# Kernel optimization log

Measured on AMD Instinct MI355X. Metric: run time of the kernel, lower is better.

## Reference

```python
import jax, jax.numpy as jnp
import numpy as np

N_NODES = 2048
N_EDGES = 49152
R_MAX = 6.0
NUM_BASIS = 8
N_LAYERS = 4
AVG_NEIGH = 24.0
MUL_S, MUL_V = 32, 16                 # hidden irreps = 32x0e + 16x1o
N_SC_OUT = MUL_S + MUL_V              # 48 scalar channels before gate (32 scalars + 16 gates)
HID = MUL_S + 3 * MUL_V               # 80 = hidden feature dim
RAD_H = 64
# tp path weight sizes: (0e x 0e -> 0e), (1o x 1o -> 0e), (0e x 1o -> 1o), (1o x 0e -> 1o), (1o x 2e -> 1o)
N1 = MUL_S * N_SC_OUT; N2 = MUL_V * N_SC_OUT; N3 = MUL_S * MUL_V; N4 = MUL_V * MUL_V; N5 = MUL_V * MUL_V
WNUM = N1 + N2 + N3 + N4 + N5         # 3328

# orthonormal symmetric-traceless basis for real l=2 (order: xy, yz, z2, xz, x2-y2)
_s2 = 1.0 / np.sqrt(2.0); _s6 = 1.0 / np.sqrt(6.0)
_Q = np.zeros((5, 3, 3), np.float32)
_Q[0, 0, 1] = _Q[0, 1, 0] = _s2
_Q[1, 1, 2] = _Q[1, 2, 1] = _s2
_Q[2, 0, 0] = _Q[2, 1, 1] = -_s6; _Q[2, 2, 2] = 2 * _s6
_Q[3, 0, 2] = _Q[3, 2, 0] = _s2
_Q[4, 0, 0] = _s2; _Q[4, 1, 1] = -_s2
Q2 = jnp.asarray(_Q)


def _sph(d):
    # component-normalized real spherical harmonics of unit vectors d [E,3]
    x, y, z = d[:, 0], d[:, 1], d[:, 2]
    y1 = jnp.sqrt(3.0) * d
    c = jnp.sqrt(15.0)
    y2 = jnp.stack([c * x * y, c * y * z, 0.5 * jnp.sqrt(5.0) * (3 * z * z - 1.0),
                    c * x * z, 0.5 * c * (x * x - y * y)], -1)
    return y1, y2


def _bessel_cutoff(r):
    # Bessel radial basis * polynomial cutoff (p=6); r [E,1]
    n = jnp.arange(1, NUM_BASIS + 1, dtype=jnp.float32)
    rbf = jnp.sqrt(2.0 / R_MAX) * jnp.sin(n * jnp.pi * r / R_MAX) / r
    u = r / R_MAX
    f = (1.0 - 28.0 * u ** 6 + 48.0 * u ** 7 - 21.0 * u ** 8) * (u < 1.0)
    return rbf * f


def _lin(h, Ws, Wv):
    # e3nn Linear hidden -> hidden (per-irrep channel mixing, fan-in normalized)
    s = h[:, :MUL_S] @ Ws / jnp.sqrt(float(MUL_S))
    v = jnp.einsum('nui,uw->nwi', h[:, MUL_S:].reshape(-1, MUL_V, 3), Wv) / jnp.sqrt(float(MUL_V))
    return jnp.concatenate([s, v.reshape(-1, 3 * MUL_V)], -1)


def reference(x, pos, edge_index, embed_w, proj_w, lin_ws, lin_wv, sc_ws, sc_wv,
              mlp_w1, mlp_b1, mlp_w2, mlp_b2, mlp_w3, mlp_b3):
    src, dst = edge_index[0], edge_index[1]
    rel = pos[dst] - pos[src]                                   # pos_i - pos_j
    r = jnp.maximum(jnp.linalg.norm(rel, axis=-1, keepdims=True), 1e-6)
    d = rel / r
    y1, y2 = _sph(d)
    rbf = _bessel_cutoff(r)                                     # [E, 8]
    # embed: only 0e->0e path exists; 1o part starts at zero
    h = jnp.concatenate([x @ embed_w / jnp.sqrt(16.0),
                         jnp.zeros((x.shape[0], 3 * MUL_V), x.dtype)], -1)
    for l in range(N_LAYERS):
        x_res = h
        x_self = _lin(h, sc_ws[l], sc_wv[l])
        hx = _lin(h, lin_ws[l], lin_wv[l])
        # radial MLP -> per-edge tensor-product weights
        f = jax.nn.silu(rbf @ mlp_w1[l] + mlp_b1[l])
        f = jax.nn.silu(f @ mlp_w2[l] + mlp_b2[l])
        w = f @ mlp_w3[l] + mlp_b3[l]                           # [E, WNUM]
        o = 0
        w1 = w[:, o:o + N1].reshape(-1, MUL_S, N_SC_OUT); o += N1
        w2 = w[:, o:o + N2].reshape(-1, MUL_V, N_SC_OUT); o += N2
        w3 = w[:, o:o + N3].reshape(-1, MUL_S, MUL_V);    o += N3
        w4 = w[:, o:o + N4].reshape(-1, MUL_V, MUL_V);    o += N4
        w5 = w[:, o:o + N5].reshape(-1, MUL_V, MUL_V)
        s_j = hx[src, :MUL_S]
        v_j = hx[src, MUL_S:].reshape(-1, MUL_V, 3)
        # scalar outputs: (0e x 0e -> 0e) and (1o x 1o -> 0e)
        p2 = jnp.einsum('eui,ei->eu', v_j, y1) / jnp.sqrt(3.0)
        out_s = (jnp.einsum('eu,euw->ew', s_j, w1) + jnp.einsum('eu,euw->ew', p2, w2)) / jnp.sqrt(48.0)
        # vector outputs: (0e x 1o -> 1o), (1o x 0e -> 1o), (1o x 2e -> 1o)
        q3 = jnp.einsum('eu,ei->eui', s_j, y1)
        q5 = jnp.sqrt(3.0 / 5.0) * jnp.einsum('eui,em,mij->euj', v_j, y2, Q2)
        out_v = (jnp.einsum('eui,euw->ewi', q3, w3) + jnp.einsum('eui,euw->ewi', v_j, w4)
                 + jnp.einsum('eui,euw->ewi', q5, w5)) / jnp.sqrt(64.0)
        msg = jnp.concatenate([out_s, out_v.reshape(-1, 3 * MUL_V)], -1)   # [E, 96]
        agg = jax.ops.segment_sum(msg, dst, num_segments=N_NODES) / jnp.sqrt(AVG_NEIGH)
        # Gate: silu on scalars, sigmoid gates scale 1o channels
        sc = jax.nn.silu(agg[:, :MUL_S])
        g = jax.nn.sigmoid(agg[:, MUL_S:MUL_S + MUL_V])
        vec = agg[:, MUL_S + MUL_V:].reshape(-1, MUL_V, 3) * g[:, :, None]
        h = x_res + x_self + jnp.concatenate([sc, vec.reshape(-1, 3 * MUL_V)], -1)
    return h[:, :MUL_S] @ proj_w / jnp.sqrt(float(MUL_S))


def setup_inputs() -> dict:
    key = jax.random.key(0)
    ks = jax.random.split(key, 16)
    nrm = jax.random.normal
    return {
        'x': nrm(ks[0], (N_NODES, 16), jnp.float32),
        'pos': 2.0 * nrm(ks[1], (N_NODES, 3), jnp.float32),
        'edge_index': jax.random.randint(ks[2], (2, N_EDGES), 0, N_NODES),
        'embed_w': nrm(ks[3], (16, MUL_S), jnp.float32),
        'proj_w': nrm(ks[4], (MUL_S, 32), jnp.float32),
        'lin_ws': nrm(ks[5], (N_LAYERS, MUL_S, MUL_S), jnp.float32),
        'lin_wv': nrm(ks[6], (N_LAYERS, MUL_V, MUL_V), jnp.float32),
        'sc_ws': nrm(ks[7], (N_LAYERS, MUL_S, MUL_S), jnp.float32),
        'sc_wv': nrm(ks[8], (N_LAYERS, MUL_V, MUL_V), jnp.float32),
        'mlp_w1': nrm(ks[9], (N_LAYERS, NUM_BASIS, RAD_H), jnp.float32) / np.sqrt(NUM_BASIS),
        'mlp_b1': jnp.zeros((N_LAYERS, RAD_H), jnp.float32),
        'mlp_w2': nrm(ks[10], (N_LAYERS, RAD_H, RAD_H), jnp.float32) / np.sqrt(RAD_H),
        'mlp_b2': jnp.zeros((N_LAYERS, RAD_H), jnp.float32),
        'mlp_w3': nrm(ks[11], (N_LAYERS, RAD_H, WNUM), jnp.float32) / np.sqrt(RAD_H),
        'mlp_b3': jnp.zeros((N_LAYERS, WNUM), jnp.float32),
    }
```

## Files before the change

kernel.cpp:

```cpp
#include <hip/hip_runtime.h>
#include <math.h>

#define NN 2048
#define NE 49152
#define WNUM 3328

typedef __attribute__((ext_vector_type(8))) _Float16 half8;
typedef __attribute__((ext_vector_type(4))) float f32x4;

__device__ __forceinline__ float silu_f(float x){ return x / (1.0f + expf(-x)); }
__device__ __forceinline__ float sigm_f(float x){ return 1.0f / (1.0f + expf(-x)); }

__global__ void geom_kernel(const float* __restrict__ pos, const int* __restrict__ ei,
                            float* __restrict__ egeo, int* __restrict__ cnt) {
  int e = blockIdx.x * 256 + threadIdx.x;
  if (e >= NE) return;
  int s = ei[e], d = ei[NE + e];
  atomicAdd(&cnt[d], 1);
  float rx = pos[d*3+0] - pos[s*3+0];
  float ry = pos[d*3+1] - pos[s*3+1];
  float rz = pos[d*3+2] - pos[s*3+2];
  float r = sqrtf(rx*rx + ry*ry + rz*rz);
  r = fmaxf(r, 1e-6f);
  float x = rx / r, y = ry / r, z = rz / r;
  const float s3 = 1.7320508075688772f;
  const float c15 = 3.872983346207417f;
  float y2_0 = c15 * x * y;
  float y2_1 = c15 * y * z;
  float y2_2 = 1.118033988749895f * (3.0f*z*z - 1.0f);
  float y2_3 = c15 * x * z;
  float y2_4 = 1.9364916731037085f * (x*x - y*y);
  const float q2 = 0.7071067811865476f;
  const float q6 = 0.4082482904638631f;
  float* g = egeo + (size_t)e * 20;
  g[0] = s3 * x; g[1] = s3 * y; g[2] = s3 * z;
  g[3+0] = -q6*y2_2 + q2*y2_4;
  g[3+1] =  q2*y2_0;
  g[3+2] =  q2*y2_3;
  g[3+3] =  q2*y2_0;
  g[3+4] = -q6*y2_2 - q2*y2_4;
  g[3+5] =  q2*y2_1;
  g[3+6] =  q2*y2_3;
  g[3+7] =  q2*y2_1;
  g[3+8] =  2.0f*q6*y2_2;
  float u = r / 6.0f;
  float fc = 0.0f;
  if (u < 1.0f) {
    float u2=u*u, u3=u2*u, u6=u3*u3, u7=u6*u, u8=u7*u;
    fc = 1.0f - 28.0f*u6 + 48.0f*u7 - 21.0f*u8;
  }
  const float pref = 0.5773502691896258f;
  const float pi6 = 0.5235987755982988f;
  #pragma unroll
  for (int n = 1; n <= 8; n++) {
    g[12 + n - 1] = pref * sinf((float)n * pi6 * r) / r * fc;
  }
}

__global__ void scan_kernel(const int* __restrict__ cnt, int* __restrict__ offs,
                            int* __restrict__ cursor) {
  __shared__ int part[256];
  int t = threadIdx.x;
  int local[8];
  int s = 0;
  #pragma unroll
  for (int j = 0; j < 8; j++) { local[j] = s; s += cnt[t*8 + j]; }
  part[t] = s;
  __syncthreads();
  for (int off = 1; off < 256; off <<= 1) {
    int v = part[t];
    int add = (t >= off) ? part[t - off] : 0;
    __syncthreads();
    part[t] = v + add;
    __syncthreads();
  }
  int excl = (t == 0) ? 0 : part[t-1];
  #pragma unroll
  for (int j = 0; j < 8; j++) {
    int o = excl + local[j];
    offs[t*8 + j] = o;
    cursor[t*8 + j] = o;
  }
  if (t == 255) offs[2048] = part[255];
}

__global__ void scatter_kernel(const int* __restrict__ ei, int* __restrict__ cursor,
                               int* __restrict__ epos) {
  int e = blockIdx.x * 256 + threadIdx.x;
  if (e >= NE) return;
  int d = ei[NE + e];
  int p = atomicAdd(&cursor[d], 1);
  epos[e] = p;
}

__global__ void conv_w3_kernel(const float* __restrict__ w3g, _Float16* __restrict__ w3h) {
  int tid = blockIdx.x * 256 + threadIdx.x;
  if (tid >= 16 * WNUM) return;
  int n = tid % WNUM;
  int lq = tid / WNUM;
  int quad = lq & 3, l = lq >> 2;
  const float* src = w3g + (size_t)l * 64 * WNUM + n;
  int idx = n >> 4, L = n & 15;
  _Float16* dst = w3h + ((size_t)(l * 208 + idx) * 2) * 512 + (quad*16 + L) * 8;
  half8 h0, h1;
  #pragma unroll
  for (int j = 0; j < 8; j++) {
    h0[j] = (_Float16)src[(size_t)(quad*8 + j) * WNUM];
    h1[j] = (_Float16)src[(size_t)(32 + quad*8 + j) * WNUM];
  }
  *(half8*)(dst)       = h0;
  *(half8*)(dst + 512) = h1;
}

#define NBR1 (NE/16)
__global__ void radial_all_kernel(const float* __restrict__ egeo,
                                  const float* __restrict__ w1, const float* __restrict__ b1,
                                  const float* __restrict__ w2, const float* __restrict__ b2,
                                  _Float16* __restrict__ f_h) {
  __shared__ float h1s[16][64];
  int l = blockIdx.x / NBR1;
  int bb = blockIdx.x % NBR1;
  int ty = threadIdx.x >> 6, dk = threadIdx.x & 63;
  int e0b = bb * 16 + ty * 4;
  const float* w1l = w1 + (size_t)l * 8 * 64;
  const float* w2l = w2 + (size_t)l * 64 * 64;
  _Float16* fl = f_h + (size_t)l * NE * 64;
  float b1v = b1[l*64 + dk];
  #pragma unroll
  for (int k = 0; k < 4; ++k) {
    const float* rb = egeo + (size_t)(e0b + k) * 20 + 12;
    float acc = b1v;
    #pragma unroll
    for (int j = 0; j < 8; j++) acc += rb[j] * w1l[j*64 + dk];
    h1s[ty*4 + k][dk] = silu_f(acc);
  }
  __syncthreads();
  float b2v = b2[l*64 + dk];
  float o0 = b2v, o1 = b2v, o2 = b2v, o3 = b2v;
  #pragma unroll 8
  for (int j = 0; j < 64; ++j) {
    float w = w2l[j*64 + dk];
    o0 += h1s[ty*4+0][j] * w;
    o1 += h1s[ty*4+1][j] * w;
    o2 += h1s[ty*4+2][j] * w;
    o3 += h1s[ty*4+3][j] * w;
  }
  fl[(size_t)(e0b+0)*64 + dk] = (_Float16)silu_f(o0);
  fl[(size_t)(e0b+1)*64 + dk] = (_Float16)silu_f(o1);
  fl[(size_t)(e0b+2)*64 + dk] = (_Float16)silu_f(o2);
  fl[(size_t)(e0b+3)*64 + dk] = (_Float16)silu_f(o3);
}

__global__ void embed_prep_kernel(const float* __restrict__ x, const float* __restrict__ ew,
                                  const float* __restrict__ lws0, const float* __restrict__ sws0,
                                  float* __restrict__ h, float* __restrict__ hx,
                                  float* __restrict__ xself) {
  __shared__ float hs[8][32];
  int t = threadIdx.x;
  int nl = t >> 5, c = t & 31;
  int n = blockIdx.x * 8 + nl;
  float v = 0.0f;
  #pragma unroll
  for (int j = 0; j < 16; j++) v += x[n*16 + j] * ew[j*32 + c];
  v *= 0.25f;
  hs[nl][c] = v;
  h[(size_t)n*80 + c] = v;
  for (int idx = t; idx < 8*48; idx += 256) {
    int nn = blockIdx.x * 8 + idx / 48;
    h[(size_t)nn*80 + 32 + idx % 48] = 0.0f;
  }
  __syncthreads();
  for (int idx = t; idx < 2*8*80; idx += 256) {
    int which = idx / 640, r = idx % 640;
    int nl2 = r / 80, cc = r % 80;
    int n2 = blockIdx.x * 8 + nl2;
    float o = 0.0f;
    if (cc < 32) {
      const float* W = which ? sws0 : lws0;
      #pragma unroll 8
      for (int u = 0; u < 32; u++) o += hs[nl2][u] * W[u*32 + cc];
      o *= 0.17677669529663687f;
    }
    (which ? xself : hx)[(size_t)n2*80 + cc] = o;
  }
}

__launch_bounds__(256, 2)
__global__ void edge_msg_kernel(const int* __restrict__ ei, const float* __restrict__ egeo,
                                const _Float16* __restrict__ f_h,
                                const float* __restrict__ hx,
                                const _Float16* __restrict__ w3h,
                                const float* __restrict__ b3g,
                                const int* __restrict__ epos,
                                float* __restrict__ msg, int l) {
  __shared__ float smem[15616];
  __shared__ int eposS[64];
  float* sT    = smem;
  float* p2T   = smem + 2048;
  float* q3T   = smem + 3072;
  float* vT    = smem + 6144;
  float* q5T   = smem + 9216;
  float* biasL = smem + 12288;
  float* poolA = smem;
  float* poolB = smem + 3072;
  float* poolC = smem + 6144;

  const int t = threadIdx.x;
  const int e0 = blockIdx.x * 64;
  const float* b3l = b3g + (size_t)l * WNUM;

  for (int i = t; i < WNUM; i += 256) biasL[i] = b3l[i];
  if (t < 64) eposS[t] = epos[e0 + t];
  for (int idx = t; idx < 64*80; idx += 256) {
    int e = idx / 80, c = idx % 80;
    int src = ei[e0 + e];
    float val = hx[(size_t)src*80 + c];
    if (c < 32) sT[c*64 + e] = val; else vT[(c-32)*64 + e] = val;
  }
  __syncthreads();
  for (int idx = t; idx < 64*16; idx += 256) {
    int u = idx >> 6, e = idx & 63;
    const float* g = &egeo[(size_t)(e0+e)*20];
    float a = vT[(u*3)*64+e]*g[0] + vT[(u*3+1)*64+e]*g[1] + vT[(u*3+2)*64+e]*g[2];
    p2T[u*64 + e] = a * 0.5773502691896258f;
  }
  for (int idx = t; idx < 64*48; idx += 256) {
    int o = idx >> 6, e = idx & 63;
    int u = o / 3, jj = o % 3;
    const float* g = &egeo[(size_t)(e0+e)*20];
    q3T[o*64 + e] = sT[u*64 + e] * g[jj];
    float a = vT[(u*3)*64+e]*g[3+jj] + vT[(u*3+1)*64+e]*g[6+jj] + vT[(u*3+2)*64+e]*g[9+jj];
    q5T[o*64 + e] = a * 0.7745966692414834f;
  }

  const int wv = t >> 6, lane = t & 63, L = lane & 15, quad = lane >> 4;
  const int qb = quad * 4;

  half8 Ah[4][2];
  #pragma unroll
  for (int g = 0; g < 4; ++g) {
    const half8* fA = (const half8*)(f_h + (size_t)(e0 + g*16 + L)*64);
    Ah[g][0] = fA[quad];
    Ah[g][1] = fA[4 + quad];
  }
  __syncthreads();

  const _Float16* wb = w3h + (size_t)l * 208 * 1024 + lane * 8;
  half8 pb0[4], pb1[4];
  float bs[4];

#define PRIME(START)                                                          \
  { _Pragma("unroll")                                                         \
    for (int _s = 0; _s < 4; ++_s) {                                          \
      const _Float16* _wn = wb + (size_t)((START) + _s) * 1024;               \
      pb0[_s] = *(const half8*)_wn;                                           \
      pb1[_s] = *(const half8*)(_wn + 512);                                   \
      bs[_s] = biasL[((START) + _s)*16 + L];                                  \
    } }

#define GCORE(IDX, CO, OKCOND)                                                \
  f32x4 a0, a1, a2, a3;                                                       \
  { half8 _B0 = pb0[(CO)&3], _B1 = pb1[(CO)&3];                               \
    float _bb = bs[(CO)&3];                                                   \
    if (OKCOND) {                                                             \
      const _Float16* _wn = wb + (size_t)((IDX) + 4) * 1024;                  \
      pb0[(CO)&3] = *(const half8*)_wn;                                       \
      pb1[(CO)&3] = *(const half8*)(_wn + 512);                               \
      bs[(CO)&3] = biasL[((IDX) + 4)*16 + L];                                 \
    }                                                                         \
    a0 = (f32x4){_bb,_bb,_bb,_bb}; a1 = a0; a2 = a0; a3 = a0;                 \
    a0 = __builtin_amdgcn_mfma_f32_16x16x32_f16(Ah[0][0], _B0, a0, 0,0,0);    \
    a0 = __builtin_amdgcn_mfma_f32_16x16x32_f16(Ah[0][1], _B1, a0, 0,0,0);    \
    a1 = __builtin_amdgcn_mfma_f32_16x16x32_f16(Ah[1][0], _B0, a1, 0,0,0);    \
    a1 = __builtin_amdgcn_mfma_f32_16x16x32_f16(Ah[1][1], _B1, a1, 0,0,0);    \
    a2 = __builtin_amdgcn_mfma_f32_16x16x32_f16(Ah[2][0], _B0, a2, 0,0,0);    \
    a2 = __builtin_amdgcn_mfma_f32_16x16x32_f16(Ah[2][1], _B1, a2, 0,0,0);    \
    a3 = __builtin_amdgcn_mfma_f32_16x16x32_f16(Ah[3][0], _B0, a3, 0,0,0);    \
    a3 = __builtin_amdgcn_mfma_f32_16x16x32_f16(Ah[3][1], _B1, a3, 0,0,0);    \
  }

  const float S48 = 0.14433756729740645f;
  const float S64 = 0.125f;

  if (wv <= 1) {
    f32x4 ms[4][3];
    #pragma unroll
    for (int g = 0; g < 4; ++g)
      #pragma unroll
      for (int j = 0; j < 3; ++j) ms[g][j] = (f32x4){0,0,0,0};
    const int ustart = wv * 16, istart = wv * 48, iend = istart + 48;
    PRIME(istart);
    for (int u4 = 0; u4 < 16; u4 += 4) {
      #pragma unroll
      for (int uu = 0; uu < 4; ++uu) {
        const int u = u4 + uu;
        f32x4 f0 = *(const f32x4*)&sT[(ustart+u)*64 + qb];
        f32x4 f1 = *(const f32x4*)&sT[(ustart+u)*64 + 16 + qb];
        f32x4 f2 = *(const f32x4*)&sT[(ustart+u)*64 + 32 + qb];
        f32x4 f3 = *(const f32x4*)&sT[(ustart+u)*64 + 48 + qb];
        #pragma unroll
        for (int j = 0; j < 3; ++j) {
          const int CO = uu*3 + j;
          const int idx = istart + u4*3 + CO;
          GCORE(idx, CO, idx + 4 < iend);
          ms[0][j] += f0*a0; ms[1][j] += f1*a1; ms[2][j] += f2*a2; ms[3][j] += f3*a3;
        }
      }
    }
    float* pool = (wv == 0) ? poolA : poolB;
    __syncthreads();
    #pragma unroll
    for (int g = 0; g < 4; ++g)
      #pragma unroll
      for (int j = 0; j < 3; ++j)
        #pragma unroll
        for (int r = 0; r < 4; ++r)
          pool[(g*16 + qb + r)*48 + j*16 + L] = ms[g][j][r];
    __syncthreads();
  } else if (wv == 2) {
    f32x4 ms[4][3], mv[4][3];
    #pragma unroll
    for (int g = 0; g < 4; ++g)
      #pragma unroll
      for (int j = 0; j < 3; ++j) { ms[g][j] = (f32x4){0,0,0,0}; mv[g][j] = (f32x4){0,0,0,0}; }
    PRIME(96);
    for (int u4 = 0; u4 < 16; u4 += 4) {
      #pragma unroll
      for (int uu = 0; uu < 4; ++uu) {
        const int u = u4 + uu;
        f32x4 f0 = *(const f32x4*)&p2T[u*64 + qb];
        f32x4 f1 = *(const f32x4*)&p2T[u*64 + 16 + qb];
        f32x4 f2 = *(const f32x4*)&p2T[u*64 + 32 + qb];
        f32x4 f3 = *(const f32x4*)&p2T[u*64 + 48 + qb];
        #pragma unroll
        for (int j = 0; j < 3; ++j) {
          const int CO = uu*3 + j;
          const int idx = 96 + u4*3 + CO;
          GCORE(idx, CO, idx + 4 < 144);
          ms[0][j] += f0*a0; ms[1][j] += f1*a1; ms[2][j] += f2*a2; ms[3][j] += f3*a3;
        }
      }
    }
    PRIME(176);
    for (int u4 = 0; u4 < 16; u4 += 4) {
      #pragma unroll
      for (int uu = 0; uu < 4; ++uu) {
        const int u = u4 + uu;
        const int idx = 176 + u;
        GCORE(idx, uu, idx + 4 < 192);
        #pragma unroll
        for (int i = 0; i < 3; ++i) {
          mv[0][i] += *(const f32x4*)&vT[(u*3+i)*64 + qb]      * a0;
          mv[1][i] += *(const f32x4*)&vT[(u*3+i)*64 + 16 + qb] * a1;
          mv[2][i] += *(const f32x4*)&vT[(u*3+i)*64 + 32 + qb] * a2;
          mv[3][i] += *(const f32x4*)&vT[(u*3+i)*64 + 48 + qb] * a3;
        }
      }
    }
    __syncthreads();
    #pragma unroll
    for (int g = 0; g < 4; ++g)
      #pragma unroll
      for (int i = 0; i < 3; ++i)
        #pragma unroll
        for (int r = 0; r < 4; ++r)
          poolC[(g*16 + qb + r)*48 + i*16 + L] = mv[g][i][r];
    __syncthreads();
    #pragma unroll
    for (int g = 0; g < 4; ++g) {
      #pragma unroll
      for (int r = 0; r < 4; ++r) {
        const int eb = g*16 + qb + r;
        float* mp = msg + (size_t)eposS[eb]*96;
        #pragma unroll
        for (int j = 0; j < 3; ++j)
          mp[j*16 + L] = (ms[g][j][r] + poolA[eb*48 + j*16 + L] + poolB[eb*48 + j*16 + L]) * S48;
      }
    }
  } else {
    f32x4 mv[4][3];
    #pragma unroll
    for (int g = 0; g < 4; ++g)
      #pragma unroll
      for (int i = 0; i < 3; ++i) mv[g][i] = (f32x4){0,0,0,0};
    PRIME(144);
    for (int u4 = 0; u4 < 32; u4 += 4) {
      #pragma unroll
      for (int uu = 0; uu < 4; ++uu) {
        const int u = u4 + uu;
        const int idx = 144 + u;
        GCORE(idx, uu, idx + 4 < 176);
        #pragma unroll
        for (int i = 0; i < 3; ++i) {
          mv[0][i] += *(const f32x4*)&q3T[(u*3+i)*64 + qb]      * a0;
          mv[1][i] += *(const f32x4*)&q3T[(u*3+i)*64 + 16 + qb] * a1;
          mv[2][i] += *(const f32x4*)&q3T[(u*3+i)*64 + 32 + qb] * a2;
          mv[3][i] += *(const f32x4*)&q3T[(u*3+i)*64 + 48 + qb] * a3;
        }
      }
    }
    PRIME(192);
    for (int u4 = 0; u4 < 16; u4 += 4) {
      #pragma unroll
      for (int uu = 0; uu < 4; ++uu) {
        const int u = u4 + uu;
        const int idx = 192 + u;
        GCORE(idx, uu, idx + 4 < 208);
        #pragma unroll
        for (int i = 0; i < 3; ++i) {
          mv[0][i] += *(const f32x4*)&q5T[(u*3+i)*64 + qb]      * a0;
          mv[1][i] += *(const f32x4*)&q5T[(u*3+i)*64 + 16 + qb] * a1;
          mv[2][i] += *(const f32x4*)&q5T[(u*3+i)*64 + 32 + qb] * a2;
          mv[3][i] += *(const f32x4*)&q5T[(u*3+i)*64 + 48 + qb] * a3;
        }
      }
    }
    __syncthreads();
    __syncthreads();
    #pragma unroll
    for (int g = 0; g < 4; ++g) {
      #pragma unroll
      for (int r = 0; r < 4; ++r) {
        const int eb = g*16 + qb + r;
        float* mp = msg + (size_t)eposS[eb]*96;
        #pragma unroll
        for (int i = 0; i < 3; ++i)
          mp[48 + 3*L + i] = (mv[g][i][r] + poolC[eb*48 + i*16 + L]) * S64;
      }
    }
  }
#undef GCORE
#undef PRIME
}

__global__ void agg_fused_kernel(const float* __restrict__ msg, const int* __restrict__ offs,
                                 const float* __restrict__ xself_in, float* __restrict__ h,
                                 const float* __restrict__ lwsN, const float* __restrict__ lwvN,
                                 const float* __restrict__ swsN, const float* __restrict__ swvN,
                                 float* __restrict__ hx_out, float* __restrict__ xself_out,
                                 const float* __restrict__ pw, float* __restrict__ out,
                                 int last) {
  __shared__ float sagg[4][96];
  __shared__ float hnew[4][80];
  int t = threadIdx.x;
  int nb = blockIdx.x * 4;
  for (int idx = t; idx < 4*96; idx += 256) {
    int nl = idx / 96, c = idx % 96;
    int n = nb + nl;
    int b = offs[n], e = offs[n+1];
    float acc = 0.0f, acc2 = 0.0f;
    int j = b;
    for (; j + 1 < e; j += 2) {
      acc  += msg[(size_t)j*96 + c];
      acc2 += msg[(size_t)(j+1)*96 + c];
    }
    if (j < e) acc += msg[(size_t)j*96 + c];
    sagg[nl][c] = (acc + acc2) * 0.20412414523193154f;
  }
  __syncthreads();
  for (int idx = t; idx < 4*80; idx += 256) {
    int nl = idx / 80, c = idx % 80;
    int n = nb + nl;
    float a;
    if (c < 32) {
      a = silu_f(sagg[nl][c]);
    } else {
      int oc = c - 32, wch = oc / 3;
      a = sagg[nl][48 + oc] * sigm_f(sagg[nl][32 + wch]);
    }
    float hn = h[(size_t)n*80 + c] + xself_in[(size_t)n*80 + c] + a;
    hnew[nl][c] = hn;
    h[(size_t)n*80 + c] = hn;
  }
  __syncthreads();
  if (!last) {
    for (int idx = t; idx < 2*4*80; idx += 256) {
      int which = idx / 320, r = idx % 320;
      int nl = r / 80, c = r % 80;
      int n = nb + nl;
      const float* Ws = which ? swsN : lwsN;
      const float* Wv = which ? swvN : lwvN;
      float v = 0.0f;
      if (c < 32) {
        #pragma unroll 8
        for (int u = 0; u < 32; u++) v += hnew[nl][u] * Ws[u*32 + c];
        v *= 0.17677669529663687f;
      } else {
        int oc = c - 32, wch = oc / 3, i = oc % 3;
        #pragma unroll
        for (int u = 0; u < 16; u++) v += hnew[nl][32 + u*3 + i] * Wv[u*16 + wch];
        v *= 0.25f;
      }
      (which ? xself_out : hx_out)[(size_t)n*80 + c] = v;
    }
  } else {
    for (int idx = t; idx < 4*32; idx += 256) {
      int nl = idx / 32, c = idx % 32;
      int n = nb + nl;
      float acc = 0.0f;
      #pragma unroll 8
      for (int u = 0; u < 32; u++) acc += hnew[nl][u] * pw[u*32 + c];
      out[(size_t)n*32 + c] = acc * 0.17677669529663687f;
    }
  }
}

extern "C" void kernel_launch(void* const* d_in, const int* in_sizes, int n_in,
                              void* d_out, int out_size, void* d_ws, size_t ws_size,
                              hipStream_t stream) {
  const float* x       = (const float*)d_in[0];
  const float* pos     = (const float*)d_in[1];
  const int*   ei      = (const int*)  d_in[2];
  const float* embed_w = (const float*)d_in[3];
  const float* proj_w  = (const float*)d_in[4];
  const float* lin_ws  = (const float*)d_in[5];
  const float* lin_wv  = (const float*)d_in[6];
  const float* sc_ws   = (const float*)d_in[7];
  const float* sc_wv   = (const float*)d_in[8];
  const float* mlp_w1  = (const float*)d_in[9];
  const float* mlp_b1  = (const float*)d_in[10];
  const float* mlp_w2  = (const float*)d_in[11];
  const float* mlp_b2  = (const float*)d_in[12];
  const float* mlp_w3  = (const float*)d_in[13];
  const float* mlp_b3  = (const float*)d_in[14];
  float* out = (float*)d_out;

  float* ws    = (float*)d_ws;
  float* egeo  = ws;
  float* h     = egeo  + (size_t)NE*20;
  float* hx    = h     + (size_t)NN*80;
  float* xself = hx    + (size_t)NN*80;
  float* msg   = xself + (size_t)NN*80;
  _Float16* f_h = (_Float16*)(msg + (size_t)NE*96);
  _Float16* w3h = f_h + (size_t)4*NE*64;
  int* cnt    = (int*)(w3h + (size_t)4*208*1024);
  int* offs   = cnt + NN;
  int* cursor = offs + NN + 1;
  int* epos   = cursor + NN;

  hipMemsetAsync(cnt, 0, NN*sizeof(int), stream);
  geom_kernel<<<(NE + 255)/256, 256, 0, stream>>>(pos, ei, egeo, cnt);
  scan_kernel<<<1, 256, 0, stream>>>(cnt, offs, cursor);
  scatter_kernel<<<NE/256, 256, 0, stream>>>(ei, cursor, epos);
  conv_w3_kernel<<<(16*WNUM + 255)/256, 256, 0, stream>>>(mlp_w3, w3h);
  radial_all_kernel<<<NBR1*4, 256, 0, stream>>>(egeo, mlp_w1, mlp_b1, mlp_w2, mlp_b2, f_h);
  embed_prep_kernel<<<NN/8, 256, 0, stream>>>(x, embed_w, lin_ws, sc_ws, h, hx, xself);

  for (int l = 0; l < 4; l++) {
    edge_msg_kernel<<<NE/64, 256, 0, stream>>>(ei, egeo, f_h + (size_t)l*NE*64, hx,
                                               w3h, mlp_b3, epos, msg, l);
    int last = (l == 3);
    agg_fused_kernel<<<NN/4, 256, 0, stream>>>(
        msg, offs, xself, h,
        lin_ws + (size_t)(l+1 < 4 ? l+1 : 0) * 1024,
        lin_wv + (size_t)(l+1 < 4 ? l+1 : 0) * 256,
        sc_ws  + (size_t)(l+1 < 4 ? l+1 : 0) * 1024,
        sc_wv  + (size_t)(l+1 < 4 ? l+1 : 0) * 256,
        hx, xself, proj_w, out, last);
  }
}
```

Baseline: 460.1 us.

## Compute radial MLP second layer with fp16 MFMA instead of scalar FMA

New measurement: 448.2 us. 1.03x faster.

```diff
diff --git a/kernel.cpp b/kernel.cpp
--- a/kernel.cpp
+++ b/kernel.cpp
@@ -112,43 +112,68 @@
   *(half8*)(dst + 512) = h1;
 }
 
-#define NBR1 (NE/16)
-__global__ void radial_all_kernel(const float* __restrict__ egeo,
-                                  const float* __restrict__ w1, const float* __restrict__ b1,
-                                  const float* __restrict__ w2, const float* __restrict__ b2,
-                                  _Float16* __restrict__ f_h) {
-  __shared__ float h1s[16][64];
-  int l = blockIdx.x / NBR1;
-  int bb = blockIdx.x % NBR1;
-  int ty = threadIdx.x >> 6, dk = threadIdx.x & 63;
-  int e0b = bb * 16 + ty * 4;
-  const float* w1l = w1 + (size_t)l * 8 * 64;
-  const float* w2l = w2 + (size_t)l * 64 * 64;
+__global__ void conv_w2_kernel(const float* __restrict__ w2g, _Float16* __restrict__ w2h) {
+  int tid = blockIdx.x * 256 + threadIdx.x;
+  if (tid >= 16384) return;
+  int j = tid & 7, lane = (tid >> 3) & 63, plane = (tid >> 9) & 1;
+  int ct = (tid >> 10) & 3, l = tid >> 12;
+  int q = lane >> 4, Lc = lane & 15;
+  int k = plane*32 + q*8 + j;
+  int n = ct*16 + Lc;
+  w2h[tid] = (_Float16)w2g[(size_t)l*4096 + k*64 + n];
+}
+
+__global__ void radial_mfma_kernel(const float* __restrict__ egeo,
+                                   const float* __restrict__ w1, const float* __restrict__ b1,
+                                   const float* __restrict__ b2,
+                                   const _Float16* __restrict__ w2h,
+                                   _Float16* __restrict__ f_h) {
+  __shared__ _Float16 h1s[64*72];
+  const int t = threadIdx.x;
+  const int l = blockIdx.x / (NE/64);
+  const int e0 = (blockIdx.x % (NE/64)) * 64;
+  const float* w1l = w1 + (size_t)l * 512;
   _Float16* fl = f_h + (size_t)l * NE * 64;
-  float b1v = b1[l*64 + dk];
-  #pragma unroll
-  for (int k = 0; k < 4; ++k) {
-    const float* rb = egeo + (size_t)(e0b + k) * 20 + 12;
-    float acc = b1v;
-    #pragma unroll
-    for (int j = 0; j < 8; j++) acc += rb[j] * w1l[j*64 + dk];
-    h1s[ty*4 + k][dk] = silu_f(acc);
-  }
-  __syncthreads();
-  float b2v = b2[l*64 + dk];
-  float o0 = b2v, o1 = b2v, o2 = b2v, o3 = b2v;
-  #pragma unroll 8
-  for (int j = 0; j < 64; ++j) {
-    float w = w2l[j*64 + dk];
-    o0 += h1s[ty*4+0][j] * w;
-    o1 += h1s[ty*4+1][j] * w;
-    o2 += h1s[ty*4+2][j] * w;
-    o3 += h1s[ty*4+3][j] * w;
-  }
-  fl[(size_t)(e0b+0)*64 + dk] = (_Float16)silu_f(o0);
-  fl[(size_t)(e0b+1)*64 + dk] = (_Float16)silu_f(o1);
-  fl[(size_t)(e0b+2)*64 + dk] = (_Float16)silu_f(o2);
-  fl[(size_t)(e0b+3)*64 + dk] = (_Float16)silu_f(o3);
+
+  {
+    int e = t >> 2, jb = (t & 3) * 16;
+    const float* rb = egeo + (size_t)(e0 + e) * 20 + 12;
+    float r0 = rb[0], r1 = rb[1], r2 = rb[2], r3 = rb[3];
+    float r4 = rb[4], r5 = rb[5], r6 = rb[6], r7 = rb[7];
+    #pragma unroll
+    for (int jj = 0; jj < 16; ++jj) {
+      int j = jb + jj;
+      float acc = b1[l*64 + j];
+      acc += r0 * w1l[0*64 + j];
+      acc += r1 * w1l[1*64 + j];
+      acc += r2 * w1l[2*64 + j];
+      acc += r3 * w1l[3*64 + j];
+      acc += r4 * w1l[4*64 + j];
+      acc += r5 * w1l[5*64 + j];
+      acc += r6 * w1l[6*64 + j];
+      acc += r7 * w1l[7*64 + j];
+      h1s[e*72 + j] = (_Float16)silu_f(acc);
+    }
+  }
+  __syncthreads();
+
+  const int wv = t >> 6, lane = t & 63, L = lane & 15, quad = lane >> 4;
+  half8 A0 = *(const half8*)&h1s[(wv*16 + L)*72 + quad*8];
+  half8 A1 = *(const half8*)&h1s[(wv*16 + L)*72 + 32 + quad*8];
+  #pragma unroll
+  for (int ct = 0; ct < 4; ++ct) {
+    const _Float16* wB = w2h + ((size_t)(l*4 + ct) * 2) * 512 + lane*8;
+    half8 B0 = *(const half8*)(wB);
+    half8 B1 = *(const half8*)(wB + 512);
+    float bb = b2[l*64 + ct*16 + L];
+    f32x4 acc = {bb, bb, bb, bb};
+    acc = __builtin_amdgcn_mfma_f32_16x16x32_f16(A0, B0, acc, 0, 0, 0);
+    acc = __builtin_amdgcn_mfma_f32_16x16x32_f16(A1, B1, acc, 0, 0, 0);
+    #pragma unroll
+    for (int r = 0; r < 4; ++r) {
+      fl[(size_t)(e0 + wv*16 + quad*4 + r)*64 + ct*16 + L] = (_Float16)silu_f(acc[r]);
+    }
+  }
 }
 
 __global__ void embed_prep_kernel(const float* __restrict__ x, const float* __restrict__ ew,
@@ -533,7 +558,8 @@
   float* msg   = xself + (size_t)NN*80;
   _Float16* f_h = (_Float16*)(msg + (size_t)NE*96);
   _Float16* w3h = f_h + (size_t)4*NE*64;
-  int* cnt    = (int*)(w3h + (size_t)4*208*1024);
+  _Float16* w2h = w3h + (size_t)4*208*1024;
+  int* cnt    = (int*)(w2h + 16384);
   int* offs   = cnt + NN;
   int* cursor = offs + NN + 1;
   int* epos   = cursor + NN;
@@ -543,7 +569,8 @@
   scan_kernel<<<1, 256, 0, stream>>>(cnt, offs, cursor);
   scatter_kernel<<<NE/256, 256, 0, stream>>>(ei, cursor, epos);
   conv_w3_kernel<<<(16*WNUM + 255)/256, 256, 0, stream>>>(mlp_w3, w3h);
-  radial_all_kernel<<<NBR1*4, 256, 0, stream>>>(egeo, mlp_w1, mlp_b1, mlp_w2, mlp_b2, f_h);
+  conv_w2_kernel<<<64, 256, 0, stream>>>(mlp_w2, w2h);
+  radial_mfma_kernel<<<4*(NE/64), 256, 0, stream>>>(egeo, mlp_w1, mlp_b1, mlp_b2, w2h, f_h);
   embed_prep_kernel<<<NN/8, 256, 0, stream>>>(x, embed_w, lin_ws, sc_ws, h, hx, xself);
 
   for (int l = 0; l < 4; l++) {
```
